# Kernel tuning notes

Hardware: AMD Instinct MI355X
Metric: run time of the kernel (lower is better)

Reference implementation:

```python
import jax, jax.numpy as jnp
import numpy as np

B, D, H, W, C = 2, 8, 64, 64, 128
NH = 8
WS = (2, 8, 8)
SS = (1, 4, 4)
HEAD_DIM = C // NH
SCALE = HEAD_DIM ** -0.5
MLP_HIDDEN = 4 * C


def _window_partition(x, ws):
    # x: (B, D, H, W, C) -> (B*nW, ws0*ws1*ws2, C)
    b, d, h, w, c = x.shape
    x = x.reshape(b, d // ws[0], ws[0], h // ws[1], ws[1], w // ws[2], ws[2], c)
    return x.transpose(0, 1, 3, 5, 2, 4, 6, 7).reshape(-1, ws[0] * ws[1] * ws[2], c)


def _window_reverse(win, ws, b, d, h, w):
    x = win.reshape(b, d // ws[0], h // ws[1], w // ws[2], ws[0], ws[1], ws[2], -1)
    return x.transpose(0, 1, 4, 2, 5, 3, 6, 7).reshape(b, d, h, w, -1)


def _rel_pos_index(ws):
    coords = np.stack(np.meshgrid(np.arange(ws[0]), np.arange(ws[1]), np.arange(ws[2]), indexing='ij'))
    cf = coords.reshape(3, -1)                       # (3, N)
    rel = (cf[:, :, None] - cf[:, None, :]).transpose(1, 2, 0)  # (N, N, 3)
    rel[:, :, 0] += ws[0] - 1
    rel[:, :, 1] += ws[1] - 1
    rel[:, :, 2] += ws[2] - 1
    rel[:, :, 0] *= (2 * ws[1] - 1) * (2 * ws[2] - 1)
    rel[:, :, 1] *= 2 * ws[2] - 1
    return rel.sum(-1)                               # (N, N)


def _attn_mask(d, h, w, ws, ss):
    img = np.zeros((1, d, h, w, 1), np.float32)
    cnt = 0
    for sd in (slice(-ws[0]), slice(-ws[0], -ss[0]), slice(-ss[0], None)):
        for sh in (slice(-ws[1]), slice(-ws[1], -ss[1]), slice(-ss[1], None)):
            for sw in (slice(-ws[2]), slice(-ws[2], -ss[2]), slice(-ss[2], None)):
                img[:, sd, sh, sw, :] = cnt
                cnt += 1
    mw = _window_partition(img, ws)[..., 0]          # (nW, N)
    am = mw[:, None, :] - mw[:, :, None]             # (nW, N, N)
    return np.where(am != 0, -100.0, 0.0).astype(np.float32)


def _ln(x, g, b):
    m = x.mean(-1, keepdims=True)
    v = ((x - m) ** 2).mean(-1, keepdims=True)
    return (x - m) / jnp.sqrt(v + 1e-5) * g + b


def setup_inputs() -> dict:
    key = jax.random.key(0)
    ks = jax.random.split(key, 8)
    n_bias = (2 * WS[0] - 1) * (2 * WS[1] - 1) * (2 * WS[2] - 1)
    return {
        'x': jax.random.normal(ks[0], (B, D, H, W, C), jnp.float32),
        'qkv_w': jax.random.normal(ks[1], (3 * C, C), jnp.float32) * 0.02,
        'qkv_b': jnp.zeros((3 * C,), jnp.float32),
        'proj_w': jax.random.normal(ks[2], (C, C), jnp.float32) * 0.02,
        'proj_b': jnp.zeros((C,), jnp.float32),
        'rpb': jax.random.normal(ks[3], (n_bias, NH), jnp.float32) * 0.02,
        'ln1_g': jnp.ones((C,), jnp.float32),
        'ln1_b': jnp.zeros((C,), jnp.float32),
        'ln2_g': jnp.ones((C,), jnp.float32),
        'ln2_b': jnp.zeros((C,), jnp.float32),
        'fc1_w': jax.random.normal(ks[4], (MLP_HIDDEN, C), jnp.float32) * 0.02,
        'fc1_b': jnp.zeros((MLP_HIDDEN,), jnp.float32),
        'fc2_w': jax.random.normal(ks[5], (C, MLP_HIDDEN), jnp.float32) * 0.02,
        'fc2_b': jnp.zeros((C,), jnp.float32),
    }


def reference(x, qkv_w, qkv_b, proj_w, proj_b, rpb, ln1_g, ln1_b, ln2_g, ln2_b, fc1_w, fc1_b, fc2_w, fc2_b):
    shortcut = x
    xn = _ln(x, ln1_g, ln1_b)
    # cyclic shift (SW-MSA)
    xs = jnp.roll(xn, (-SS[0], -SS[1], -SS[2]), axis=(1, 2, 3))
    win = _window_partition(xs, WS)                  # (Bw, N, C)
    Bw, N, _ = win.shape
    qkv = (win @ qkv_w.T + qkv_b).reshape(Bw, N, 3, NH, HEAD_DIM).transpose(2, 0, 3, 1, 4)
    q, k, v = qkv[0] * SCALE, qkv[1], qkv[2]         # (Bw, NH, N, d)
    attn = jnp.einsum('bhnd,bhmd->bhnm', q, k)       # (Bw, NH, N, N)
    rpi = _rel_pos_index(WS)
    bias = rpb[rpi.reshape(-1)].reshape(N, N, NH).transpose(2, 0, 1)  # (NH, N, N)
    attn = attn + bias[None]
    mask = jnp.asarray(_attn_mask(D, H, W, WS, SS))  # (nW, N, N)
    nW = mask.shape[0]
    attn = attn.reshape(B, nW, NH, N, N) + mask[None, :, None]
    attn = jax.nn.softmax(attn, axis=-1).reshape(Bw, NH, N, N)
    out = jnp.einsum('bhnm,bhmd->bhnd', attn, v).transpose(0, 2, 1, 3).reshape(Bw, N, C)
    out = out @ proj_w.T + proj_b
    xr = _window_reverse(out, WS, B, D, H, W)
    xr = jnp.roll(xr, SS, axis=(1, 2, 3))
    x1 = shortcut + xr
    # MLP block
    y = _ln(x1, ln2_g, ln2_b)
    y = jax.nn.gelu(y @ fc1_w.T + fc1_b, approximate=False)
    y = y @ fc2_w.T + fc2_b
    return x1 + y
```

## Files before the change

kernel.cpp:

```cpp
#include <hip/hip_runtime.h>
#include <math.h>

typedef short s16x8 __attribute__((ext_vector_type(8)));
typedef short s16x4 __attribute__((ext_vector_type(4)));
typedef float f32x4 __attribute__((ext_vector_type(4)));

#define MFMA(a, b, c)    __builtin_amdgcn_mfma_f32_16x16x32_bf16(a, b, c, 0, 0, 0)
#define MFMA16(a, b, c)  __builtin_amdgcn_mfma_f32_16x16x16bf16_1k(a, b, c, 0, 0, 0)

__device__ __forceinline__ float b2f(ushort u) {
    union { unsigned int i; float f; } v; v.i = ((unsigned int)u) << 16; return v.f;
}
__device__ __forceinline__ ushort f2b(float f) {
    union { float f; unsigned int i; } v; v.f = f;
    unsigned int r = v.i + 0x7fffu + ((v.i >> 16) & 1u);
    return (ushort)(r >> 16);
}
__device__ __forceinline__ float gelu_tanh(float v) {
    float u = 0.7978845608f * (v + 0.044715f * v * v * v);
    float e = __expf(-2.f * fabsf(u));
    float t = (1.f - e) / (1.f + e);
    t = (u < 0.f) ? -t : t;
    return 0.5f * v * (1.f + t);
}

__global__ __launch_bounds__(256) void k0_prep(
    const float* __restrict__ qkv_w, const float* __restrict__ proj_w,
    const float* __restrict__ fc1_w, const float* __restrict__ fc2_w,
    const float* __restrict__ rpb, ushort* __restrict__ wq,
    ushort* __restrict__ wp, ushort* __restrict__ wf, ushort* __restrict__ bm)
{
    int bid = blockIdx.x, tid = threadIdx.x;
    if (bid < 192) { int idx = bid * 256 + tid; wq[idx] = f2b(qkv_w[idx]); return; }
    if (bid < 256) { int idx = (bid - 192) * 256 + tid; wp[idx] = f2b(proj_w[idx]); return; }
    if (bid < 768) {
        int idx = (bid - 256) * 256 + tid;
        wf[idx] = f2b(idx < 65536 ? fc1_w[idx] : fc2_w[idx - 65536]);
        return;
    }
    int bi = bid - 768;
    int cls = bi >> 3, head = bi & 7;
    int ed = (cls >> 2) & 1, eh = (cls >> 1) & 1, ew = cls & 1;
    int j = tid & 127;
    int tdj = j >> 6, thj = (j >> 3) & 7, twj = j & 7;
    int regj = (ed ? (tdj + 1) : 0) * 9
             + (eh ? ((thj < 4) ? 1 : 2) : 0) * 3
             + (ew ? ((twj < 4) ? 1 : 2) : 0);
    ushort* bmp = bm + (long)bi * 16384;
    for (int ii = 0; ii < 64; ++ii) {
        int i = (tid >> 7) * 64 + ii;
        int tdi = i >> 6, thi = (i >> 3) & 7, twi = i & 7;
        int regi = (ed ? (tdi + 1) : 0) * 9
                 + (eh ? ((thi < 4) ? 1 : 2) : 0) * 3
                 + (ew ? ((twi < 4) ? 1 : 2) : 0);
        int rpi = (tdi - tdj + 1) * 225 + (thi - thj + 7) * 15 + (twi - twj + 7);
        float v = rpb[rpi * 8 + head] + ((regi != regj) ? -100.f : 0.f);
        bmp[i * 128 + j] = f2b(v);
    }
}

__global__ __launch_bounds__(256) void k2_qkv(
    const float* __restrict__ x, const float* __restrict__ g,
    const float* __restrict__ be, const ushort* __restrict__ wq,
    const float* __restrict__ qkv_b, ushort* __restrict__ qkv)
{
    __shared__ __align__(16) ushort As[128][136];
    int tid = threadIdx.x;
    int m0 = blockIdx.x * 128;
    {
        int row = tid >> 1, half = tid & 1;
        int tk = m0 + row;
        int wi = tk >> 7, t = tk & 127;
        int b = wi >> 8, wd = (wi >> 6) & 3, wh = (wi >> 3) & 7, ww = wi & 7;
        int td = t >> 6, th = (t >> 3) & 7, tw = t & 7;
        int d = (wd * 2 + td + 1) & 7;
        int h = (wh * 8 + th + 4) & 63;
        int w = (ww * 8 + tw + 4) & 63;
        long src = (((long)((b * 8 + d) * 64 + h)) * 64 + w) * 128 + half * 64;
        float vals[64];
        float s = 0.f, q = 0.f;
        #pragma unroll
        for (int i = 0; i < 16; ++i) {
            float4 u = *(const float4*)&x[src + i * 4];
            vals[i * 4 + 0] = u.x; vals[i * 4 + 1] = u.y;
            vals[i * 4 + 2] = u.z; vals[i * 4 + 3] = u.w;
            s += u.x + u.y + u.z + u.w;
            q += u.x * u.x + u.y * u.y + u.z * u.z + u.w * u.w;
        }
        s += __shfl_xor(s, 1);
        q += __shfl_xor(q, 1);
        float mean = s * (1.f / 128.f);
        float rstd = rsqrtf(q * (1.f / 128.f) - mean * mean + 1e-5f);
        #pragma unroll
        for (int i = 0; i < 8; ++i) {
            ushort pk[8];
            #pragma unroll
            for (int jj = 0; jj < 8; ++jj) {
                int c = half * 64 + i * 8 + jj;
                pk[jj] = f2b((vals[i * 8 + jj] - mean) * rstd * g[c] + be[c]);
            }
            *(uint4*)&As[row][half * 64 + i * 8] = *(uint4*)pk;
        }
    }
    __syncthreads();
    int wv = tid >> 6, lane = tid & 63, li = lane & 15, quad = lane >> 4;
    int wm = wv >> 1, wn = wv & 1;
    long wibase = (long)(m0 >> 7) * 49152;
    for (int nb = 0; nb < 3; ++nb) {
        f32x4 acc[4][4] = {};
        for (int s = 0; s < 4; ++s) {
            s16x8 a[4], bw[4];
            #pragma unroll
            for (int mi = 0; mi < 4; ++mi)
                a[mi] = *(const s16x8*)&As[wm * 64 + mi * 16 + li][s * 32 + quad * 8];
            #pragma unroll
            for (int ni = 0; ni < 4; ++ni)
                bw[ni] = *(const s16x8*)&wq[(long)(nb * 128 + wn * 64 + ni * 16 + li) * 128
                                            + s * 32 + quad * 8];
            #pragma unroll
            for (int mi = 0; mi < 4; ++mi)
                #pragma unroll
                for (int ni = 0; ni < 4; ++ni)
                    acc[mi][ni] = MFMA(a[mi], bw[ni], acc[mi][ni]);
        }
        #pragma unroll
        for (int mi = 0; mi < 4; ++mi)
            #pragma unroll
            for (int ni = 0; ni < 4; ++ni) {
                int gcol = nb * 128 + wn * 64 + ni * 16 + li;
                int mat = gcol >> 7, hd = (gcol >> 4) & 7;
                float bias = qkv_b[gcol];
                float scale = (mat == 0) ? 0.25f : 1.f;
                long base2 = wibase + mat * 16384 + hd * 2048 + li;
                #pragma unroll
                for (int r = 0; r < 4; ++r) {
                    int trow = wm * 64 + mi * 16 + quad * 4 + r;
                    qkv[base2 + trow * 16] = f2b((acc[mi][ni][r] + bias) * scale);
                }
            }
    }
}

__global__ __launch_bounds__(64) void k3_attn(
    ushort* __restrict__ qkv, const ushort* __restrict__ bm)
{
    __shared__ __align__(16) ushort vt[16][136];
    int b = blockIdx.x;
    int wi = b >> 2, qq = b & 3;
    int wd = (wi >> 6) & 3, wh = (wi >> 3) & 7, ww = wi & 7;
    int cls = ((wd == 3) << 2) | ((wh == 7) << 1) | (ww == 7);
    int lane = threadIdx.x;
    int li = lane & 15, quad = lane >> 4;
    long wbase = (long)wi * 49152;
    int row0 = qq * 32;
    for (int h = 0; h < 8; ++h) {
        __syncthreads();
        #pragma unroll
        for (int t2 = 0; t2 < 2; ++t2) {
            int tok = t2 * 64 + lane;
            const ushort* vp = &qkv[wbase + 32768 + h * 2048 + tok * 16];
            uint4 v0 = *(const uint4*)vp;
            uint4 v1 = *(const uint4*)(vp + 8);
            const ushort* p0 = (const ushort*)&v0;
            const ushort* p1 = (const ushort*)&v1;
            #pragma unroll
            for (int j = 0; j < 8; ++j) { vt[j][tok] = p0[j]; vt[8 + j][tok] = p1[j]; }
        }
        __syncthreads();
        s16x4 qf0 = *(const s16x4*)&qkv[wbase + h * 2048 + (row0 + li) * 16 + quad * 4];
        s16x4 qf1 = *(const s16x4*)&qkv[wbase + h * 2048 + (row0 + 16 + li) * 16 + quad * 4];
        long bmb = (long)(cls * 8 + h) * 16384;
        float ps0 = 0.f, ps1 = 0.f;
        uint pa0[8][2], pa1[8][2];
        #pragma unroll
        for (int mi = 0; mi < 8; ++mi) {
            s16x4 kf = *(const s16x4*)&qkv[wbase + 16384 + h * 2048 + (mi * 16 + li) * 16 + quad * 4];
            f32x4 z = {0.f, 0.f, 0.f, 0.f};
            f32x4 s0 = MFMA16(kf, qf0, z);
            f32x4 s1 = MFMA16(kf, qf1, z);
            s16x4 b0 = *(const s16x4*)&bm[bmb + (row0 + li) * 128 + mi * 16 + quad * 4];
            s16x4 b1 = *(const s16x4*)&bm[bmb + (row0 + 16 + li) * 128 + mi * 16 + quad * 4];
            float e0 = __expf(s0[0] + b2f((ushort)b0[0]));
            float e1 = __expf(s0[1] + b2f((ushort)b0[1]));
            float e2 = __expf(s0[2] + b2f((ushort)b0[2]));
            float e3 = __expf(s0[3] + b2f((ushort)b0[3]));
            ps0 += (e0 + e1) + (e2 + e3);
            pa0[mi][0] = (uint)f2b(e0) | ((uint)f2b(e1) << 16);
            pa0[mi][1] = (uint)f2b(e2) | ((uint)f2b(e3) << 16);
            float f0 = __expf(s1[0] + b2f((ushort)b1[0]));
            float f1 = __expf(s1[1] + b2f((ushort)b1[1]));
            float f2 = __expf(s1[2] + b2f((ushort)b1[2]));
            float f3 = __expf(s1[3] + b2f((ushort)b1[3]));
            ps1 += (f0 + f1) + (f2 + f3);
            pa1[mi][0] = (uint)f2b(f0) | ((uint)f2b(f1) << 16);
            pa1[mi][1] = (uint)f2b(f2) | ((uint)f2b(f3) << 16);
        }
        ps0 += __shfl_xor(ps0, 16); ps0 += __shfl_xor(ps0, 32);
        ps1 += __shfl_xor(ps1, 16); ps1 += __shfl_xor(ps1, 32);
        float inv0 = 1.f / ps0, inv1 = 1.f / ps1;
        f32x4 pc0 = {0.f, 0.f, 0.f, 0.f}, pc1 = {0.f, 0.f, 0.f, 0.f};
        #pragma unroll
        for (int mi = 0; mi < 8; ++mi) {
            s16x4 vf = *(const s16x4*)&vt[li][mi * 16 + quad * 4];
            union { uint2 u; s16x4 v; } a0, a1;
            a0.u.x = pa0[mi][0]; a0.u.y = pa0[mi][1];
            a1.u.x = pa1[mi][0]; a1.u.y = pa1[mi][1];
            pc0 = MFMA16(a0.v, vf, pc0);
            pc1 = MFMA16(a1.v, vf, pc1);
        }
        #pragma unroll
        for (int r = 0; r < 4; ++r) {
            float oi0 = __shfl(inv0, quad * 4 + r);
            float oi1 = __shfl(inv1, quad * 4 + r);
            int i0 = row0 + quad * 4 + r;
            int i1 = row0 + 16 + quad * 4 + r;
            qkv[wbase + h * 2048 + (long)i0 * 16 + li] = f2b(pc0[r] * oi0);
            qkv[wbase + h * 2048 + (long)i1 * 16 + li] = f2b(pc1[r] * oi1);
        }
    }
}

__global__ __launch_bounds__(256) void k45(
    const ushort* __restrict__ ao, const ushort* __restrict__ wp,
    const float* __restrict__ proj_b, const float* __restrict__ x,
    const float* __restrict__ g2, const float* __restrict__ be2,
    const ushort* __restrict__ wf1, const float* __restrict__ fc1_b,
    const ushort* __restrict__ wf2, const float* __restrict__ fc2_b,
    float* __restrict__ out)
{
    __shared__ __align__(16) ushort As[64][132];
    __shared__ __align__(16) ushort hs[64][132];
    __shared__ float redS[2][64];
    __shared__ float redQ[2][64];
    int tid = threadIdx.x;
    int b = blockIdx.x;
    int wi = b >> 1, half64 = b & 1;
    int wd = (wi >> 6) & 3, wh = (wi >> 3) & 7, ww = wi & 7;
    int bb = wi >> 8;
    long aob = (long)wi * 49152;
    int tok0 = half64 * 64;
    #pragma unroll
    for (int i = 0; i < 4; ++i) {
        int slot = tid + i * 256;
        int row = slot & 63, hsl = slot >> 6;
        *(uint4*)&As[row][hsl * 8] =
            *(const uint4*)&ao[aob + (hsl >> 1) * 2048 + (long)(tok0 + row) * 16 + (hsl & 1) * 8];
    }
    __syncthreads();
    int wv = tid >> 6, lane = tid & 63, li = lane & 15, quad = lane >> 4;
    int wm = wv >> 1, wn = wv & 1;
    f32x4 acc[2][4] = {};
    for (int s = 0; s < 4; ++s) {
        s16x8 a[2], bw[4];
        #pragma unroll
        for (int mi = 0; mi < 2; ++mi)
            a[mi] = *(const s16x8*)&As[wm * 32 + mi * 16 + li][s * 32 + quad * 8];
        #pragma unroll
        for (int ni = 0; ni < 4; ++ni)
            bw[ni] = *(const s16x8*)&wp[(long)(wn * 64 + ni * 16 + li) * 128 + s * 32 + quad * 8];
        #pragma unroll
        for (int mi = 0; mi < 2; ++mi)
            #pragma unroll
            for (int ni = 0; ni < 4; ++ni)
                acc[mi][ni] = MFMA(a[mi], bw[ni], acc[mi][ni]);
    }
    int cols[4];
    #pragma unroll
    for (int ni = 0; ni < 4; ++ni) cols[ni] = wn * 64 + ni * 16 + li;
    {
        float pbv[4];
        #pragma unroll
        for (int ni = 0; ni < 4; ++ni) pbv[ni] = proj_b[cols[ni]];
        #pragma unroll
        for (int mi = 0; mi < 2; ++mi) {
            #pragma unroll
            for (int r = 0; r < 4; ++r) {
                int lrow = wm * 32 + mi * 16 + quad * 4 + r;
                int t = half64 * 64 + lrow;
                int td = t >> 6, th = (t >> 3) & 7, tw = t & 7;
                int d = (wd * 2 + td + 1) & 7, h = (wh * 8 + th + 4) & 63, w = (ww * 8 + tw + 4) & 63;
                long di = (((long)((bb * 8 + d) * 64 + h)) * 64 + w) * 128;
                float s_ = 0.f, q_ = 0.f;
                #pragma unroll
                for (int ni = 0; ni < 4; ++ni) {
                    float v = acc[mi][ni][r] + pbv[ni] + x[di + cols[ni]];
                    acc[mi][ni][r] = v;
                    s_ += v; q_ += v * v;
                }
                #pragma unroll
                for (int m = 1; m < 16; m <<= 1) {
                    s_ += __shfl_xor(s_, m);
                    q_ += __shfl_xor(q_, m);
                }
                if (li == 0) { redS[wn][lrow] = s_; redQ[wn][lrow] = q_; }
            }
        }
    }
    __syncthreads();
    {
        float g2v[4], be2v[4];
        #pragma unroll
        for (int ni = 0; ni < 4; ++ni) { g2v[ni] = g2[cols[ni]]; be2v[ni] = be2[cols[ni]]; }
        #pragma unroll
        for (int mi = 0; mi < 2; ++mi) {
            #pragma unroll
            for (int r = 0; r < 4; ++r) {
                int lrow = wm * 32 + mi * 16 + quad * 4 + r;
                float tS = redS[0][lrow] + redS[1][lrow];
                float tQ = redQ[0][lrow] + redQ[1][lrow];
                float mean = tS * (1.f / 128.f);
                float rstd = rsqrtf(tQ * (1.f / 128.f) - mean * mean + 1e-5f);
                #pragma unroll
                for (int ni = 0; ni < 4; ++ni)
                    As[lrow][cols[ni]] = f2b((acc[mi][ni][r] - mean) * rstd * g2v[ni] + be2v[ni]);
            }
        }
    }
    uint x1p[2][4][2];
    #pragma unroll
    for (int mi = 0; mi < 2; ++mi)
        #pragma unroll
        for (int ni = 0; ni < 4; ++ni)
            #pragma unroll
            for (int rr = 0; rr < 2; ++rr)
                x1p[mi][ni][rr] = (unsigned int)f2b(acc[mi][ni][2 * rr])
                                | ((unsigned int)f2b(acc[mi][ni][2 * rr + 1]) << 16);
    __syncthreads();
    f32x4 yacc[2][4] = {};
    for (int hc = 0; hc < 4; ++hc) {
        f32x4 hacc[2][4] = {};
        #pragma unroll
        for (int kk = 0; kk < 4; ++kk) {
            s16x8 a[2], bw[4];
            #pragma unroll
            for (int mi = 0; mi < 2; ++mi)
                a[mi] = *(const s16x8*)&As[wm * 32 + mi * 16 + li][kk * 32 + quad * 8];
            #pragma unroll
            for (int ni = 0; ni < 4; ++ni)
                bw[ni] = *(const s16x8*)&wf1[(long)(hc * 128 + wn * 64 + ni * 16 + li) * 128
                                             + kk * 32 + quad * 8];
            #pragma unroll
            for (int mi = 0; mi < 2; ++mi)
                #pragma unroll
                for (int ni = 0; ni < 4; ++ni)
                    hacc[mi][ni] = MFMA(a[mi], bw[ni], hacc[mi][ni]);
        }
        #pragma unroll
        for (int mi = 0; mi < 2; ++mi)
            #pragma unroll
            for (int ni = 0; ni < 4; ++ni) {
                int col = wn * 64 + ni * 16 + li;
                float bbv = fc1_b[hc * 128 + col];
                #pragma unroll
                for (int r = 0; r < 4; ++r) {
                    int row = wm * 32 + mi * 16 + quad * 4 + r;
                    hs[row][col] = f2b(gelu_tanh(hacc[mi][ni][r] + bbv));
                }
            }
        __syncthreads();
        #pragma unroll
        for (int kk = 0; kk < 4; ++kk) {
            s16x8 a[2], bw[4];
            #pragma unroll
            for (int mi = 0; mi < 2; ++mi)
                a[mi] = *(const s16x8*)&hs[wm * 32 + mi * 16 + li][kk * 32 + quad * 8];
            #pragma unroll
            for (int ni = 0; ni < 4; ++ni)
                bw[ni] = *(const s16x8*)&wf2[(long)(wn * 64 + ni * 16 + li) * 512
                                             + hc * 128 + kk * 32 + quad * 8];
            #pragma unroll
            for (int mi = 0; mi < 2; ++mi)
                #pragma unroll
                for (int ni = 0; ni < 4; ++ni)
                    yacc[mi][ni] = MFMA(a[mi], bw[ni], yacc[mi][ni]);
        }
        __syncthreads();
    }
    {
        float f2v[4];
        #pragma unroll
        for (int ni = 0; ni < 4; ++ni) f2v[ni] = fc2_b[cols[ni]];
        #pragma unroll
        for (int mi = 0; mi < 2; ++mi) {
            #pragma unroll
            for (int r = 0; r < 4; ++r) {
                int lrow = wm * 32 + mi * 16 + quad * 4 + r;
                int t = half64 * 64 + lrow;
                int td = t >> 6, th = (t >> 3) & 7, tw = t & 7;
                int d = (wd * 2 + td + 1) & 7, h = (wh * 8 + th + 4) & 63, w = (ww * 8 + tw + 4) & 63;
                long di = (((long)((bb * 8 + d) * 64 + h)) * 64 + w) * 128;
                #pragma unroll
                for (int ni = 0; ni < 4; ++ni) {
                    unsigned int wrd = x1p[mi][ni][r >> 1];
                    float x1v = b2f((ushort)((wrd >> ((r & 1) * 16)) & 0xffffu));
                    out[di + cols[ni]] = x1v + yacc[mi][ni][r] + f2v[ni];
                }
            }
        }
    }
}

extern "C" void kernel_launch(void* const* d_in, const int* in_sizes, int n_in,
                              void* d_out, int out_size, void* d_ws, size_t ws_size,
                              hipStream_t stream)
{
    (void)in_sizes; (void)n_in; (void)out_size; (void)ws_size;
    const float* x      = (const float*)d_in[0];
    const float* qkv_w  = (const float*)d_in[1];
    const float* qkv_b  = (const float*)d_in[2];
    const float* proj_w = (const float*)d_in[3];
    const float* proj_b = (const float*)d_in[4];
    const float* rpb    = (const float*)d_in[5];
    const float* ln1_g  = (const float*)d_in[6];
    const float* ln1_b  = (const float*)d_in[7];
    const float* ln2_g  = (const float*)d_in[8];
    const float* ln2_b  = (const float*)d_in[9];
    const float* fc1_w  = (const float*)d_in[10];
    const float* fc1_b  = (const float*)d_in[11];
    const float* fc2_w  = (const float*)d_in[12];
    const float* fc2_b  = (const float*)d_in[13];
    float* out = (float*)d_out;

    ushort* qkvb = (ushort*)d_ws;
    ushort* wq   = (ushort*)((char*)d_ws + 50331648);
    ushort* wp   = wq + 49152;
    ushort* wf   = wp + 16384;
    ushort* bm   = wf + 131072;

    hipLaunchKernelGGL(k0_prep, dim3(832), dim3(256), 0, stream,
                       qkv_w, proj_w, fc1_w, fc2_w, rpb, wq, wp, wf, bm);
    hipLaunchKernelGGL(k2_qkv, dim3(512), dim3(256), 0, stream,
                       x, ln1_g, ln1_b, wq, qkv_b, qkvb);
    hipLaunchKernelGGL(k3_attn, dim3(2048), dim3(64), 0, stream, qkvb, bm);
    hipLaunchKernelGGL(k45, dim3(1024), dim3(256), 0, stream,
                       qkvb, wp, proj_b, x, ln2_g, ln2_b,
                       wf, fc1_b, wf + 65536, fc2_b, out);
}
```

Before: 310.1 us.

## Split attention heads across blocks and process whole windows per MLP block

The attention kernel now gives each (window, query-quarter, head) triple its own 64-thread block, replacing the serial loop over 8 heads. This launches 8x more waves to hide memory and exp latency, and removes the per-head barriers. The fused proj/LN/MLP kernel now handles all 128 tokens of a window in one 512-thread block instead of two 64-token halves. This halves how often each weight tile is reread per window, at the cost of doubling LDS per block and halving the block count.

```diff
diff --git a/kernel.cpp b/kernel.cpp
--- a/kernel.cpp
+++ b/kernel.cpp
@@ -146,81 +146,78 @@
 {
     __shared__ __align__(16) ushort vt[16][136];
     int b = blockIdx.x;
-    int wi = b >> 2, qq = b & 3;
+    int h = b & 7, qq = (b >> 3) & 3, wi = b >> 5;
     int wd = (wi >> 6) & 3, wh = (wi >> 3) & 7, ww = wi & 7;
     int cls = ((wd == 3) << 2) | ((wh == 7) << 1) | (ww == 7);
     int lane = threadIdx.x;
     int li = lane & 15, quad = lane >> 4;
-    long wbase = (long)wi * 49152;
+    long hb = (long)wi * 49152 + h * 2048;
     int row0 = qq * 32;
-    for (int h = 0; h < 8; ++h) {
-        __syncthreads();
-        #pragma unroll
-        for (int t2 = 0; t2 < 2; ++t2) {
-            int tok = t2 * 64 + lane;
-            const ushort* vp = &qkv[wbase + 32768 + h * 2048 + tok * 16];
-            uint4 v0 = *(const uint4*)vp;
-            uint4 v1 = *(const uint4*)(vp + 8);
-            const ushort* p0 = (const ushort*)&v0;
-            const ushort* p1 = (const ushort*)&v1;
-            #pragma unroll
-            for (int j = 0; j < 8; ++j) { vt[j][tok] = p0[j]; vt[8 + j][tok] = p1[j]; }
-        }
-        __syncthreads();
-        s16x4 qf0 = *(const s16x4*)&qkv[wbase + h * 2048 + (row0 + li) * 16 + quad * 4];
-        s16x4 qf1 = *(const s16x4*)&qkv[wbase + h * 2048 + (row0 + 16 + li) * 16 + quad * 4];
-        long bmb = (long)(cls * 8 + h) * 16384;
-        float ps0 = 0.f, ps1 = 0.f;
-        uint pa0[8][2], pa1[8][2];
-        #pragma unroll
-        for (int mi = 0; mi < 8; ++mi) {
-            s16x4 kf = *(const s16x4*)&qkv[wbase + 16384 + h * 2048 + (mi * 16 + li) * 16 + quad * 4];
-            f32x4 z = {0.f, 0.f, 0.f, 0.f};
-            f32x4 s0 = MFMA16(kf, qf0, z);
-            f32x4 s1 = MFMA16(kf, qf1, z);
-            s16x4 b0 = *(const s16x4*)&bm[bmb + (row0 + li) * 128 + mi * 16 + quad * 4];
-            s16x4 b1 = *(const s16x4*)&bm[bmb + (row0 + 16 + li) * 128 + mi * 16 + quad * 4];
-            float e0 = __expf(s0[0] + b2f((ushort)b0[0]));
-            float e1 = __expf(s0[1] + b2f((ushort)b0[1]));
-            float e2 = __expf(s0[2] + b2f((ushort)b0[2]));
-            float e3 = __expf(s0[3] + b2f((ushort)b0[3]));
-            ps0 += (e0 + e1) + (e2 + e3);
-            pa0[mi][0] = (uint)f2b(e0) | ((uint)f2b(e1) << 16);
-            pa0[mi][1] = (uint)f2b(e2) | ((uint)f2b(e3) << 16);
-            float f0 = __expf(s1[0] + b2f((ushort)b1[0]));
-            float f1 = __expf(s1[1] + b2f((ushort)b1[1]));
-            float f2 = __expf(s1[2] + b2f((ushort)b1[2]));
-            float f3 = __expf(s1[3] + b2f((ushort)b1[3]));
-            ps1 += (f0 + f1) + (f2 + f3);
-            pa1[mi][0] = (uint)f2b(f0) | ((uint)f2b(f1) << 16);
-            pa1[mi][1] = (uint)f2b(f2) | ((uint)f2b(f3) << 16);
-        }
-        ps0 += __shfl_xor(ps0, 16); ps0 += __shfl_xor(ps0, 32);
-        ps1 += __shfl_xor(ps1, 16); ps1 += __shfl_xor(ps1, 32);
-        float inv0 = 1.f / ps0, inv1 = 1.f / ps1;
-        f32x4 pc0 = {0.f, 0.f, 0.f, 0.f}, pc1 = {0.f, 0.f, 0.f, 0.f};
-        #pragma unroll
-        for (int mi = 0; mi < 8; ++mi) {
-            s16x4 vf = *(const s16x4*)&vt[li][mi * 16 + quad * 4];
-            union { uint2 u; s16x4 v; } a0, a1;
-            a0.u.x = pa0[mi][0]; a0.u.y = pa0[mi][1];
-            a1.u.x = pa1[mi][0]; a1.u.y = pa1[mi][1];
-            pc0 = MFMA16(a0.v, vf, pc0);
-            pc1 = MFMA16(a1.v, vf, pc1);
-        }
-        #pragma unroll
-        for (int r = 0; r < 4; ++r) {
-            float oi0 = __shfl(inv0, quad * 4 + r);
-            float oi1 = __shfl(inv1, quad * 4 + r);
-            int i0 = row0 + quad * 4 + r;
-            int i1 = row0 + 16 + quad * 4 + r;
-            qkv[wbase + h * 2048 + (long)i0 * 16 + li] = f2b(pc0[r] * oi0);
-            qkv[wbase + h * 2048 + (long)i1 * 16 + li] = f2b(pc1[r] * oi1);
-        }
-    }
-}
-
-__global__ __launch_bounds__(256) void k45(
+    #pragma unroll
+    for (int t2 = 0; t2 < 2; ++t2) {
+        int tok = t2 * 64 + lane;
+        const ushort* vp = &qkv[hb + 32768 + tok * 16];
+        uint4 v0 = *(const uint4*)vp;
+        uint4 v1 = *(const uint4*)(vp + 8);
+        const ushort* p0 = (const ushort*)&v0;
+        const ushort* p1 = (const ushort*)&v1;
+        #pragma unroll
+        for (int j = 0; j < 8; ++j) { vt[j][tok] = p0[j]; vt[8 + j][tok] = p1[j]; }
+    }
+    s16x4 qf0 = *(const s16x4*)&qkv[hb + (row0 + li) * 16 + quad * 4];
+    s16x4 qf1 = *(const s16x4*)&qkv[hb + (row0 + 16 + li) * 16 + quad * 4];
+    __syncthreads();
+    long bmb = (long)(cls * 8 + h) * 16384;
+    float ps0 = 0.f, ps1 = 0.f;
+    uint pa0[8][2], pa1[8][2];
+    #pragma unroll
+    for (int mi = 0; mi < 8; ++mi) {
+        s16x4 kf = *(const s16x4*)&qkv[hb + 16384 + (mi * 16 + li) * 16 + quad * 4];
+        f32x4 z = {0.f, 0.f, 0.f, 0.f};
+        f32x4 s0 = MFMA16(kf, qf0, z);
+        f32x4 s1 = MFMA16(kf, qf1, z);
+        s16x4 b0 = *(const s16x4*)&bm[bmb + (row0 + li) * 128 + mi * 16 + quad * 4];
+        s16x4 b1 = *(const s16x4*)&bm[bmb + (row0 + 16 + li) * 128 + mi * 16 + quad * 4];
+        float e0 = __expf(s0[0] + b2f((ushort)b0[0]));
+        float e1 = __expf(s0[1] + b2f((ushort)b0[1]));
+        float e2 = __expf(s0[2] + b2f((ushort)b0[2]));
+        float e3 = __expf(s0[3] + b2f((ushort)b0[3]));
+        ps0 += (e0 + e1) + (e2 + e3);
+        pa0[mi][0] = (uint)f2b(e0) | ((uint)f2b(e1) << 16);
+        pa0[mi][1] = (uint)f2b(e2) | ((uint)f2b(e3) << 16);
+        float f0 = __expf(s1[0] + b2f((ushort)b1[0]));
+        float f1 = __expf(s1[1] + b2f((ushort)b1[1]));
+        float f2 = __expf(s1[2] + b2f((ushort)b1[2]));
+        float f3 = __expf(s1[3] + b2f((ushort)b1[3]));
+        ps1 += (f0 + f1) + (f2 + f3);
+        pa1[mi][0] = (uint)f2b(f0) | ((uint)f2b(f1) << 16);
+        pa1[mi][1] = (uint)f2b(f2) | ((uint)f2b(f3) << 16);
+    }
+    ps0 += __shfl_xor(ps0, 16); ps0 += __shfl_xor(ps0, 32);
+    ps1 += __shfl_xor(ps1, 16); ps1 += __shfl_xor(ps1, 32);
+    float inv0 = 1.f / ps0, inv1 = 1.f / ps1;
+    f32x4 pc0 = {0.f, 0.f, 0.f, 0.f}, pc1 = {0.f, 0.f, 0.f, 0.f};
+    #pragma unroll
+    for (int mi = 0; mi < 8; ++mi) {
+        s16x4 vf = *(const s16x4*)&vt[li][mi * 16 + quad * 4];
+        union { uint2 u; s16x4 v; } a0, a1;
+        a0.u.x = pa0[mi][0]; a0.u.y = pa0[mi][1];
+        a1.u.x = pa1[mi][0]; a1.u.y = pa1[mi][1];
+        pc0 = MFMA16(a0.v, vf, pc0);
+        pc1 = MFMA16(a1.v, vf, pc1);
+    }
+    #pragma unroll
+    for (int r = 0; r < 4; ++r) {
+        float oi0 = __shfl(inv0, quad * 4 + r);
+        float oi1 = __shfl(inv1, quad * 4 + r);
+        int i0 = row0 + quad * 4 + r;
+        int i1 = row0 + 16 + quad * 4 + r;
+        qkv[hb + (long)i0 * 16 + li] = f2b(pc0[r] * oi0);
+        qkv[hb + (long)i1 * 16 + li] = f2b(pc1[r] * oi1);
+    }
+}
+
+__global__ __launch_bounds__(512) void k45(
     const ushort* __restrict__ ao, const ushort* __restrict__ wp,
     const float* __restrict__ proj_b, const float* __restrict__ x,
     const float* __restrict__ g2, const float* __restrict__ be2,
@@ -228,23 +225,21 @@
     const ushort* __restrict__ wf2, const float* __restrict__ fc2_b,
     float* __restrict__ out)
 {
-    __shared__ __align__(16) ushort As[64][132];
-    __shared__ __align__(16) ushort hs[64][132];
-    __shared__ float redS[2][64];
-    __shared__ float redQ[2][64];
+    __shared__ __align__(16) ushort As[128][132];
+    __shared__ __align__(16) ushort hs[128][132];
+    __shared__ float redS[2][128];
+    __shared__ float redQ[2][128];
     int tid = threadIdx.x;
-    int b = blockIdx.x;
-    int wi = b >> 1, half64 = b & 1;
+    int wi = blockIdx.x;
     int wd = (wi >> 6) & 3, wh = (wi >> 3) & 7, ww = wi & 7;
     int bb = wi >> 8;
     long aob = (long)wi * 49152;
-    int tok0 = half64 * 64;
     #pragma unroll
     for (int i = 0; i < 4; ++i) {
-        int slot = tid + i * 256;
-        int row = slot & 63, hsl = slot >> 6;
+        int slot = tid + i * 512;
+        int row = slot & 127, hsl = slot >> 7;
         *(uint4*)&As[row][hsl * 8] =
-            *(const uint4*)&ao[aob + (hsl >> 1) * 2048 + (long)(tok0 + row) * 16 + (hsl & 1) * 8];
+            *(const uint4*)&ao[aob + (hsl >> 1) * 2048 + (long)row * 16 + (hsl & 1) * 8];
     }
     __syncthreads();
     int wv = tid >> 6, lane = tid & 63, li = lane & 15, quad = lane >> 4;
@@ -275,8 +270,7 @@
         for (int mi = 0; mi < 2; ++mi) {
             #pragma unroll
             for (int r = 0; r < 4; ++r) {
-                int lrow = wm * 32 + mi * 16 + quad * 4 + r;
-                int t = half64 * 64 + lrow;
+                int t = wm * 32 + mi * 16 + quad * 4 + r;
                 int td = t >> 6, th = (t >> 3) & 7, tw = t & 7;
                 int d = (wd * 2 + td + 1) & 7, h = (wh * 8 + th + 4) & 63, w = (ww * 8 + tw + 4) & 63;
                 long di = (((long)((bb * 8 + d) * 64 + h)) * 64 + w) * 128;
@@ -292,7 +286,7 @@
                     s_ += __shfl_xor(s_, m);
                     q_ += __shfl_xor(q_, m);
                 }
-                if (li == 0) { redS[wn][lrow] = s_; redQ[wn][lrow] = q_; }
+                if (li == 0) { redS[wn][t] = s_; redQ[wn][t] = q_; }
             }
         }
     }
@@ -305,14 +299,14 @@
         for (int mi = 0; mi < 2; ++mi) {
             #pragma unroll
             for (int r = 0; r < 4; ++r) {
-                int lrow = wm * 32 + mi * 16 + quad * 4 + r;
-                float tS = redS[0][lrow] + redS[1][lrow];
-                float tQ = redQ[0][lrow] + redQ[1][lrow];
+                int t = wm * 32 + mi * 16 + quad * 4 + r;
+                float tS = redS[0][t] + redS[1][t];
+                float tQ = redQ[0][t] + redQ[1][t];
                 float mean = tS * (1.f / 128.f);
                 float rstd = rsqrtf(tQ * (1.f / 128.f) - mean * mean + 1e-5f);
                 #pragma unroll
                 for (int ni = 0; ni < 4; ++ni)
-                    As[lrow][cols[ni]] = f2b((acc[mi][ni][r] - mean) * rstd * g2v[ni] + be2v[ni]);
+                    As[t][cols[ni]] = f2b((acc[mi][ni][r] - mean) * rstd * g2v[ni] + be2v[ni]);
             }
         }
     }
@@ -384,8 +378,7 @@
         for (int mi = 0; mi < 2; ++mi) {
             #pragma unroll
             for (int r = 0; r < 4; ++r) {
-                int lrow = wm * 32 + mi * 16 + quad * 4 + r;
-                int t = half64 * 64 + lrow;
+                int t = wm * 32 + mi * 16 + quad * 4 + r;
                 int td = t >> 6, th = (t >> 3) & 7, tw = t & 7;
                 int d = (wd * 2 + td + 1) & 7, h = (wh * 8 + th + 4) & 63, w = (ww * 8 + tw + 4) & 63;
                 long di = (((long)((bb * 8 + d) * 64 + h)) * 64 + w) * 128;
@@ -431,8 +424,8 @@
                        qkv_w, proj_w, fc1_w, fc2_w, rpb, wq, wp, wf, bm);
     hipLaunchKernelGGL(k2_qkv, dim3(512), dim3(256), 0, stream,
                        x, ln1_g, ln1_b, wq, qkv_b, qkvb);
-    hipLaunchKernelGGL(k3_attn, dim3(2048), dim3(64), 0, stream, qkvb, bm);
-    hipLaunchKernelGGL(k45, dim3(1024), dim3(256), 0, stream,
+    hipLaunchKernelGGL(k3_attn, dim3(16384), dim3(64), 0, stream, qkvb, bm);
+    hipLaunchKernelGGL(k45, dim3(512), dim3(512), 0, stream,
                        qkvb, wp, proj_b, x, ln2_g, ln2_b,
                        wf, fc1_b, wf + 65536, fc2_b, out);
 }
```

Measured after the change: 295.3 us. -4.8%, faster.

## Split attention by head per block, stage K in LDS, restructure LN2 via shared x1 tile

Applied to the files above, without the earlier changes.

The attention kernel now gives each block one (window, head) pair and loops over the four 32-row query chunks. V and K for that head are loaded into LDS once and reused across all query chunks, instead of reloading V per head and reading K from global per query chunk. The grid doubles to 4096 blocks. In the MLP kernel, the residual x1 is stored as bf16 in a shared tile, and LayerNorm2 is computed per token by four thread groups with a shared reduction. This replaces the shuffle-based reduction and the register-packed x1, lowering register pressure at the cost of more LDS.

```diff
diff --git a/kernel.cpp b/kernel.cpp
--- a/kernel.cpp
+++ b/kernel.cpp
@@ -145,36 +145,39 @@
     ushort* __restrict__ qkv, const ushort* __restrict__ bm)
 {
     __shared__ __align__(16) ushort vt[16][136];
+    __shared__ __align__(16) ushort ks[128][24];
     int b = blockIdx.x;
-    int wi = b >> 2, qq = b & 3;
+    int h = b & 7, wi = b >> 3;
     int wd = (wi >> 6) & 3, wh = (wi >> 3) & 7, ww = wi & 7;
     int cls = ((wd == 3) << 2) | ((wh == 7) << 1) | (ww == 7);
     int lane = threadIdx.x;
     int li = lane & 15, quad = lane >> 4;
-    long wbase = (long)wi * 49152;
-    int row0 = qq * 32;
-    for (int h = 0; h < 8; ++h) {
-        __syncthreads();
-        #pragma unroll
-        for (int t2 = 0; t2 < 2; ++t2) {
-            int tok = t2 * 64 + lane;
-            const ushort* vp = &qkv[wbase + 32768 + h * 2048 + tok * 16];
-            uint4 v0 = *(const uint4*)vp;
-            uint4 v1 = *(const uint4*)(vp + 8);
-            const ushort* p0 = (const ushort*)&v0;
-            const ushort* p1 = (const ushort*)&v1;
-            #pragma unroll
-            for (int j = 0; j < 8; ++j) { vt[j][tok] = p0[j]; vt[8 + j][tok] = p1[j]; }
-        }
-        __syncthreads();
-        s16x4 qf0 = *(const s16x4*)&qkv[wbase + h * 2048 + (row0 + li) * 16 + quad * 4];
-        s16x4 qf1 = *(const s16x4*)&qkv[wbase + h * 2048 + (row0 + 16 + li) * 16 + quad * 4];
-        long bmb = (long)(cls * 8 + h) * 16384;
+    long hb = (long)wi * 49152 + h * 2048;
+    #pragma unroll
+    for (int t2 = 0; t2 < 2; ++t2) {
+        int tok = t2 * 64 + lane;
+        const ushort* vp = &qkv[hb + 32768 + tok * 16];
+        uint4 v0 = *(const uint4*)vp;
+        uint4 v1 = *(const uint4*)(vp + 8);
+        const ushort* p0 = (const ushort*)&v0;
+        const ushort* p1 = (const ushort*)&v1;
+        #pragma unroll
+        for (int j = 0; j < 8; ++j) { vt[j][tok] = p0[j]; vt[8 + j][tok] = p1[j]; }
+        const ushort* kp = &qkv[hb + 16384 + tok * 16];
+        *(uint4*)&ks[tok][0] = *(const uint4*)kp;
+        *(uint4*)&ks[tok][8] = *(const uint4*)(kp + 8);
+    }
+    __syncthreads();
+    long bmb = (long)(cls * 8 + h) * 16384;
+    for (int qq = 0; qq < 4; ++qq) {
+        int row0 = qq * 32;
+        s16x4 qf0 = *(const s16x4*)&qkv[hb + (row0 + li) * 16 + quad * 4];
+        s16x4 qf1 = *(const s16x4*)&qkv[hb + (row0 + 16 + li) * 16 + quad * 4];
         float ps0 = 0.f, ps1 = 0.f;
         uint pa0[8][2], pa1[8][2];
         #pragma unroll
         for (int mi = 0; mi < 8; ++mi) {
-            s16x4 kf = *(const s16x4*)&qkv[wbase + 16384 + h * 2048 + (mi * 16 + li) * 16 + quad * 4];
+            s16x4 kf = *(const s16x4*)&ks[mi * 16 + li][quad * 4];
             f32x4 z = {0.f, 0.f, 0.f, 0.f};
             f32x4 s0 = MFMA16(kf, qf0, z);
             f32x4 s1 = MFMA16(kf, qf1, z);
@@ -214,8 +217,8 @@
             float oi1 = __shfl(inv1, quad * 4 + r);
             int i0 = row0 + quad * 4 + r;
             int i1 = row0 + 16 + quad * 4 + r;
-            qkv[wbase + h * 2048 + (long)i0 * 16 + li] = f2b(pc0[r] * oi0);
-            qkv[wbase + h * 2048 + (long)i1 * 16 + li] = f2b(pc1[r] * oi1);
+            qkv[hb + (long)i0 * 16 + li] = f2b(pc0[r] * oi0);
+            qkv[hb + (long)i1 * 16 + li] = f2b(pc1[r] * oi1);
         }
     }
 }
@@ -229,9 +232,10 @@
     float* __restrict__ out)
 {
     __shared__ __align__(16) ushort As[64][132];
+    __shared__ __align__(16) ushort x1t[64][132];
     __shared__ __align__(16) ushort hs[64][132];
-    __shared__ float redS[2][64];
-    __shared__ float redQ[2][64];
+    __shared__ float redS[4][64];
+    __shared__ float redQ[4][64];
     int tid = threadIdx.x;
     int b = blockIdx.x;
     int wi = b >> 1, half64 = b & 1;
@@ -264,67 +268,52 @@
             for (int ni = 0; ni < 4; ++ni)
                 acc[mi][ni] = MFMA(a[mi], bw[ni], acc[mi][ni]);
     }
-    int cols[4];
     #pragma unroll
-    for (int ni = 0; ni < 4; ++ni) cols[ni] = wn * 64 + ni * 16 + li;
-    {
-        float pbv[4];
-        #pragma unroll
-        for (int ni = 0; ni < 4; ++ni) pbv[ni] = proj_b[cols[ni]];
-        #pragma unroll
-        for (int mi = 0; mi < 2; ++mi) {
-            #pragma unroll
-            for (int r = 0; r < 4; ++r) {
-                int lrow = wm * 32 + mi * 16 + quad * 4 + r;
-                int t = half64 * 64 + lrow;
-                int td = t >> 6, th = (t >> 3) & 7, tw = t & 7;
-                int d = (wd * 2 + td + 1) & 7, h = (wh * 8 + th + 4) & 63, w = (ww * 8 + tw + 4) & 63;
-                long di = (((long)((bb * 8 + d) * 64 + h)) * 64 + w) * 128;
-                float s_ = 0.f, q_ = 0.f;
-                #pragma unroll
-                for (int ni = 0; ni < 4; ++ni) {
-                    float v = acc[mi][ni][r] + pbv[ni] + x[di + cols[ni]];
-                    acc[mi][ni][r] = v;
-                    s_ += v; q_ += v * v;
-                }
-                #pragma unroll
-                for (int m = 1; m < 16; m <<= 1) {
-                    s_ += __shfl_xor(s_, m);
-                    q_ += __shfl_xor(q_, m);
-                }
-                if (li == 0) { redS[wn][lrow] = s_; redQ[wn][lrow] = q_; }
+    for (int mi = 0; mi < 2; ++mi) {
+        #pragma unroll
+        for (int r = 0; r < 4; ++r) {
+            int lrow = wm * 32 + mi * 16 + quad * 4 + r;
+            int t = half64 * 64 + lrow;
+            int td = t >> 6, th = (t >> 3) & 7, tw = t & 7;
+            int d = (wd * 2 + td + 1) & 7, h = (wh * 8 + th + 4) & 63, w = (ww * 8 + tw + 4) & 63;
+            long di = (((long)((bb * 8 + d) * 64 + h)) * 64 + w) * 128;
+            #pragma unroll
+            for (int ni = 0; ni < 4; ++ni) {
+                int col = wn * 64 + ni * 16 + li;
+                x1t[lrow][col] = f2b(acc[mi][ni][r] + proj_b[col] + x[di + col]);
             }
         }
     }
     __syncthreads();
     {
-        float g2v[4], be2v[4];
-        #pragma unroll
-        for (int ni = 0; ni < 4; ++ni) { g2v[ni] = g2[cols[ni]]; be2v[ni] = be2[cols[ni]]; }
-        #pragma unroll
-        for (int mi = 0; mi < 2; ++mi) {
-            #pragma unroll
-            for (int r = 0; r < 4; ++r) {
-                int lrow = wm * 32 + mi * 16 + quad * 4 + r;
-                float tS = redS[0][lrow] + redS[1][lrow];
-                float tQ = redQ[0][lrow] + redQ[1][lrow];
-                float mean = tS * (1.f / 128.f);
-                float rstd = rsqrtf(tQ * (1.f / 128.f) - mean * mean + 1e-5f);
-                #pragma unroll
-                for (int ni = 0; ni < 4; ++ni)
-                    As[lrow][cols[ni]] = f2b((acc[mi][ni][r] - mean) * rstd * g2v[ni] + be2v[ni]);
-            }
-        }
-    }
-    uint x1p[2][4][2];
-    #pragma unroll
-    for (int mi = 0; mi < 2; ++mi)
-        #pragma unroll
-        for (int ni = 0; ni < 4; ++ni)
-            #pragma unroll
-            for (int rr = 0; rr < 2; ++rr)
-                x1p[mi][ni][rr] = (unsigned int)f2b(acc[mi][ni][2 * rr])
-                                | ((unsigned int)f2b(acc[mi][ni][2 * rr + 1]) << 16);
+        int token = tid & 63, part = tid >> 6;
+        float vals[32];
+        float s = 0.f, q = 0.f;
+        #pragma unroll
+        for (int i = 0; i < 4; ++i) {
+            uint4 u = *(const uint4*)&x1t[token][part * 32 + i * 8];
+            const ushort* p = (const ushort*)&u;
+            #pragma unroll
+            for (int j = 0; j < 8; ++j) { float f = b2f(p[j]); vals[i * 8 + j] = f; s += f; q += f * f; }
+        }
+        redS[part][token] = s; redQ[part][token] = q;
+        __syncthreads();
+        float st = 0.f, qt = 0.f;
+        #pragma unroll
+        for (int p2 = 0; p2 < 4; ++p2) { st += redS[p2][token]; qt += redQ[p2][token]; }
+        float mean = st * (1.f / 128.f);
+        float rstd = rsqrtf(qt * (1.f / 128.f) - mean * mean + 1e-5f);
+        #pragma unroll
+        for (int i = 0; i < 4; ++i) {
+            ushort packed[8];
+            #pragma unroll
+            for (int j = 0; j < 8; ++j) {
+                int c = part * 32 + i * 8 + j;
+                packed[j] = f2b((vals[i * 8 + j] - mean) * rstd * g2[c] + be2[c]);
+            }
+            *(uint4*)&As[token][part * 32 + i * 8] = *(uint4*)packed;
+        }
+    }
     __syncthreads();
     f32x4 yacc[2][4] = {};
     for (int hc = 0; hc < 4; ++hc) {
@@ -376,25 +365,19 @@
         }
         __syncthreads();
     }
-    {
-        float f2v[4];
-        #pragma unroll
-        for (int ni = 0; ni < 4; ++ni) f2v[ni] = fc2_b[cols[ni]];
-        #pragma unroll
-        for (int mi = 0; mi < 2; ++mi) {
-            #pragma unroll
-            for (int r = 0; r < 4; ++r) {
-                int lrow = wm * 32 + mi * 16 + quad * 4 + r;
-                int t = half64 * 64 + lrow;
-                int td = t >> 6, th = (t >> 3) & 7, tw = t & 7;
-                int d = (wd * 2 + td + 1) & 7, h = (wh * 8 + th + 4) & 63, w = (ww * 8 + tw + 4) & 63;
-                long di = (((long)((bb * 8 + d) * 64 + h)) * 64 + w) * 128;
-                #pragma unroll
-                for (int ni = 0; ni < 4; ++ni) {
-                    unsigned int wrd = x1p[mi][ni][r >> 1];
-                    float x1v = b2f((ushort)((wrd >> ((r & 1) * 16)) & 0xffffu));
-                    out[di + cols[ni]] = x1v + yacc[mi][ni][r] + f2v[ni];
-                }
+    #pragma unroll
+    for (int mi = 0; mi < 2; ++mi) {
+        #pragma unroll
+        for (int r = 0; r < 4; ++r) {
+            int lrow = wm * 32 + mi * 16 + quad * 4 + r;
+            int t = half64 * 64 + lrow;
+            int td = t >> 6, th = (t >> 3) & 7, tw = t & 7;
+            int d = (wd * 2 + td + 1) & 7, h = (wh * 8 + th + 4) & 63, w = (ww * 8 + tw + 4) & 63;
+            long di = (((long)((bb * 8 + d) * 64 + h)) * 64 + w) * 128;
+            #pragma unroll
+            for (int ni = 0; ni < 4; ++ni) {
+                int col = wn * 64 + ni * 16 + li;
+                out[di + col] = b2f(x1t[lrow][col]) + yacc[mi][ni][r] + fc2_b[col];
             }
         }
     }
@@ -431,7 +414,7 @@
                        qkv_w, proj_w, fc1_w, fc2_w, rpb, wq, wp, wf, bm);
     hipLaunchKernelGGL(k2_qkv, dim3(512), dim3(256), 0, stream,
                        x, ln1_g, ln1_b, wq, qkv_b, qkvb);
-    hipLaunchKernelGGL(k3_attn, dim3(2048), dim3(64), 0, stream, qkvb, bm);
+    hipLaunchKernelGGL(k3_attn, dim3(4096), dim3(64), 0, stream, qkvb, bm);
     hipLaunchKernelGGL(k45, dim3(1024), dim3(256), 0, stream,
                        qkvb, wp, proj_b, x, ln2_g, ln2_b,
                        wf, fc1_b, wf + 65536, fc2_b, out);
```

After: 283.0 us. 8.7% less time.
